# Kernel optimization log

Hardware: AMD Instinct MI355X
Metric: run time of the kernel (lower is better)

## Reference

```python
import jax, jax.numpy as jnp
import numpy as np

L = 2      # decoder layers
B = 4      # batch
T = 1000   # seq_len (mask built for this length)
C = 768    # input_dim / d_model
H = 12     # num_heads
DK = C // H
WIN = 100


def layernorm(x, g, b):
    m = x.mean(-1, keepdims=True)
    v = x.var(-1, keepdims=True)
    return (x - m) / jnp.sqrt(v + 1e-5) * g + b


def pos_encoding(t, c):
    # Transformer-XL / espnet RelPositionalEncoding table: relative positions t-1 .. -(t-1)
    rel = jnp.arange(t - 1, -t, -1, dtype=jnp.float32)          # (2t-1,)
    div = jnp.exp(-jnp.arange(0, c, 2, dtype=jnp.float32) * (np.log(10000.0) / c))
    ang = rel[:, None] * div[None, :]                            # (2t-1, c/2)
    pe = jnp.zeros((2 * t - 1, c), dtype=jnp.float32)
    pe = pe.at[:, 0::2].set(jnp.sin(ang)).at[:, 1::2].set(jnp.cos(ang))
    return pe


def rel_shift(x):
    # x: (B, H, T, 2T-1) -> (B, H, T, T), Transformer-XL relative shift
    b, h, t, p = x.shape
    xp = jnp.pad(x, ((0, 0), (0, 0), (0, 0), (1, 0)))
    xp = xp.reshape(b, h, p + 1, t)[:, :, 1:, :].reshape(b, h, t, p)
    return xp[..., :t]


def setup_inputs() -> dict:
    key = jax.random.key(0)
    ks = jax.random.split(key, 16)
    s = 0.02
    inp = {
        "x": jax.random.normal(ks[0], (B, T, C), dtype=jnp.float32),
        "Wq": jax.random.normal(ks[1], (L, C, C), dtype=jnp.float32) * s,
        "bq": jnp.zeros((L, C), dtype=jnp.float32),
        "Wk": jax.random.normal(ks[2], (L, C, C), dtype=jnp.float32) * s,
        "bk": jnp.zeros((L, C), dtype=jnp.float32),
        "Wv": jax.random.normal(ks[3], (L, C, C), dtype=jnp.float32) * s,
        "bv": jnp.zeros((L, C), dtype=jnp.float32),
        "Wo": jax.random.normal(ks[4], (L, C, C), dtype=jnp.float32) * s,
        "bo": jnp.zeros((L, C), dtype=jnp.float32),
        "Wp": jax.random.normal(ks[5], (L, C, C), dtype=jnp.float32) * s,   # linear_pos, no bias
        "pos_u": jax.random.normal(ks[6], (L, H, DK), dtype=jnp.float32) * s,
        "pos_v": jax.random.normal(ks[7], (L, H, DK), dtype=jnp.float32) * s,
        "ln1_g": jnp.ones((L, C), dtype=jnp.float32),
        "ln1_b": jnp.zeros((L, C), dtype=jnp.float32),
        "ln2_g": jnp.ones((L, C), dtype=jnp.float32),
        "ln2_b": jnp.zeros((L, C), dtype=jnp.float32),
        "W1": jax.random.normal(ks[8], (L, C, C), dtype=jnp.float32) * s,   # mlp_ratio = 1
        "b1": jnp.zeros((L, C), dtype=jnp.float32),
        "W2": jax.random.normal(ks[9], (L, C, C), dtype=jnp.float32) * s,
        "b2": jnp.zeros((L, C), dtype=jnp.float32),
    }
    # diagonal (banded) mask: True = blocked outside the attention window
    i = np.arange(T)
    blocked = np.abs(i[:, None] - i[None, :]) > (WIN // 2)
    inp["att_mask"] = jnp.asarray(blocked)
    return inp


def reference(x, att_mask, Wq, bq, Wk, bk, Wv, bv, Wo, bo, Wp, pos_u, pos_v,
              ln1_g, ln1_b, ln2_g, ln2_b, W1, b1, W2, b2):
    Bb, t, c = x.shape
    pe = pos_encoding(t, c)                       # (2T-1, C)
    h = x * jnp.sqrt(jnp.float32(c))              # xscale in RelPositionalEncoding
    for l in range(L):
        y = layernorm(h, ln1_g[l], ln1_b[l])
        q = (y @ Wq[l] + bq[l]).reshape(Bb, t, H, DK)
        k = (y @ Wk[l] + bk[l]).reshape(Bb, t, H, DK)
        v = (y @ Wv[l] + bv[l]).reshape(Bb, t, H, DK)
        p = (pe @ Wp[l]).reshape(2 * t - 1, H, DK)
        ac = jnp.einsum('bthd,bshd->bhts', q + pos_u[l], k)
        bd = rel_shift(jnp.einsum('bthd,phd->bhtp', q + pos_v[l], p))
        scores = (ac + bd) / jnp.sqrt(jnp.float32(DK))
        scores = jnp.where(att_mask[None, None], jnp.float32(-1e9), scores)
        attn = jax.nn.softmax(scores, axis=-1)
        o = jnp.einsum('bhts,bshd->bthd', attn, v).reshape(Bb, t, c)
        h = h + (o @ Wo[l] + bo[l])
        y2 = layernorm(h, ln2_g[l], ln2_b[l])
        h = h + (jax.nn.gelu(y2 @ W1[l] + b1[l]) @ W2[l] + b2[l])
    return h
```

## Files before the change

kernel.cpp:

```cpp
#include <hip/hip_runtime.h>
#include <math.h>

#define LNUM 2
#define BBATCH 4
#define TSEQ 1000
#define CDIM 768
#define HHEADS 12
#define DKK 64
#define PPOS (2*TSEQ-1)
#define HALFW 50
#define MROWS (BBATCH*TSEQ)
#define MPAD 4096
#define QKVDIM (3*CDIM)
#define NS 176

typedef __attribute__((ext_vector_type(8))) short s16x8;
typedef __attribute__((ext_vector_type(4))) short s16x4;
typedef __attribute__((ext_vector_type(4))) float f32x4;

#define LDSOFF(p) ((unsigned)(uintptr_t)(__attribute__((address_space(3))) const void*)(p))

__device__ __forceinline__ ushort f2bf(float x) {
    unsigned u = __float_as_uint(x);
    unsigned r = u + 0x7FFFu + ((u >> 16) & 1u);
    return (ushort)(r >> 16);
}
__device__ __forceinline__ float bf2f(ushort h) {
    return __uint_as_float(((unsigned)h) << 16);
}
__device__ __forceinline__ float gelu_f(float x) {
    float u = 0.7978845608028654f * (x + 0.044715f * x * x * x);
    return 0.5f * x * (1.f + tanhf(u));
}
__device__ __forceinline__ void gload_lds16(const void* g, void* l) {
    __builtin_amdgcn_global_load_lds(
        (const __attribute__((address_space(1))) void*)g,
        (__attribute__((address_space(3))) void*)l, 16, 0, 0);
}
__device__ __forceinline__ s16x4 tr_read(unsigned addr) {
    s16x4 d;
    asm volatile("ds_read_b64_tr_b16 %0, %1" : "=v"(d) : "v"(addr));
    return d;
}
__device__ __forceinline__ s16x4 tr_read128(unsigned addr) {
    s16x4 d;
    asm volatile("ds_read_b64_tr_b16 %0, %1 offset:128" : "=v"(d) : "v"(addr));
    return d;
}

__global__ __launch_bounds__(256) void transpose_pack(
    const float* __restrict__ Wq, const float* __restrict__ Wk,
    const float* __restrict__ Wv, const float* __restrict__ Wp,
    const float* __restrict__ Wo, const float* __restrict__ W1,
    const float* __restrict__ W2,
    ushort* __restrict__ Wtqkv, ushort* __restrict__ Wtp,
    ushort* __restrict__ Wto, ushort* __restrict__ Wt1, ushort* __restrict__ Wt2) {
    const int l = blockIdx.z / 7, m = blockIdx.z % 7;
    const float* srcs[7] = {Wq, Wk, Wv, Wp, Wo, W1, W2};
    const float* src = srcs[m] + (size_t)l * CDIM * CDIM;
    ushort* dst;
    if (m < 3)       dst = Wtqkv + (size_t)l * QKVDIM * CDIM + (size_t)m * CDIM * CDIM;
    else if (m == 3) dst = Wtp + (size_t)l * CDIM * CDIM;
    else if (m == 4) dst = Wto + (size_t)l * CDIM * CDIM;
    else if (m == 5) dst = Wt1 + (size_t)l * CDIM * CDIM;
    else             dst = Wt2 + (size_t)l * CDIM * CDIM;
    __shared__ float tile[32][33];
    const int tx = threadIdx.x, ty = threadIdx.y;
    const int c0 = blockIdx.x * 32, r0 = blockIdx.y * 32;
#pragma unroll
    for (int i = 0; i < 4; ++i)
        tile[ty + i * 8][tx] = src[(size_t)(r0 + ty + i * 8) * CDIM + c0 + tx];
    __syncthreads();
#pragma unroll
    for (int i = 0; i < 4; ++i)
        dst[(size_t)(c0 + ty + i * 8) * CDIM + r0 + tx] = f2bf(tile[tx][ty + i * 8]);
}

__global__ __launch_bounds__(256) void prep_small(ushort* __restrict__ pe,
                                                  const float* __restrict__ bq,
                                                  const float* __restrict__ bk,
                                                  const float* __restrict__ bv,
                                                  float* __restrict__ bqkv) {
    int idx = blockIdx.x * 256 + threadIdx.x;
    const int npair = 256 * (CDIM / 2);
    if (idx < npair) {
        int jloc = idx / (CDIM / 2);
        int m = idx - jloc * (CDIM / 2);
        int j = 896 + jloc;
        float rel = (float)(TSEQ - 1 - j);
        float div = expf(-(float)(2 * m) * (9.210340371976184f / (float)CDIM));
        float a = rel * div;
        pe[(size_t)j * CDIM + 2 * m]     = f2bf(sinf(a));
        pe[(size_t)j * CDIM + 2 * m + 1] = f2bf(cosf(a));
    }
    if (idx < LNUM * QKVDIM) {
        int l = idx / QKVDIM, c = idx - l * QKVDIM;
        float v;
        if (c < CDIM)            v = bq[l * CDIM + c];
        else if (c < 2 * CDIM)   v = bk[l * CDIM + c - CDIM];
        else                     v = bv[l * CDIM + c - 2 * CDIM];
        bqkv[idx] = v;
    }
}

__global__ __launch_bounds__(192) void ln_kernel(const float* __restrict__ in,
                                                 const float* __restrict__ g,
                                                 const float* __restrict__ bta,
                                                 ushort* __restrict__ y, float xscale) {
    const int row = blockIdx.x, tid = threadIdx.x;
    float4 v = *(const float4*)&in[(size_t)row * CDIM + tid * 4];
    v.x *= xscale; v.y *= xscale; v.z *= xscale; v.w *= xscale;
    float s  = v.x + v.y + v.z + v.w;
    float ss = v.x * v.x + v.y * v.y + v.z * v.z + v.w * v.w;
#pragma unroll
    for (int off = 32; off; off >>= 1) {
        s  += __shfl_xor(s, off);
        ss += __shfl_xor(ss, off);
    }
    __shared__ float sm[3], sq[3];
    const int wid = tid >> 6, lane = tid & 63;
    if (lane == 0) { sm[wid] = s; sq[wid] = ss; }
    __syncthreads();
    const float st  = sm[0] + sm[1] + sm[2];
    const float sst = sq[0] + sq[1] + sq[2];
    const float mean = st * (1.f / CDIM);
    const float var  = sst * (1.f / CDIM) - mean * mean;
    const float rstd = rsqrtf(var + 1e-5f);
    const float4 g4 = *(const float4*)&g[tid * 4];
    const float4 b4 = *(const float4*)&bta[tid * 4];
    ushort o0 = f2bf((v.x - mean) * rstd * g4.x + b4.x);
    ushort o1 = f2bf((v.y - mean) * rstd * g4.y + b4.y);
    ushort o2 = f2bf((v.z - mean) * rstd * g4.z + b4.z);
    ushort o3 = f2bf((v.w - mean) * rstd * g4.w + b4.w);
    uint2 pk; pk.x = (unsigned)o0 | ((unsigned)o1 << 16);
    pk.y = (unsigned)o2 | ((unsigned)o3 << 16);
    *(uint2*)&y[(size_t)row * CDIM + tid * 4] = pk;
}

template <int EPI>
__global__ __launch_bounds__(256, 3) void gemm64(const ushort* __restrict__ A,
                                                 const ushort* __restrict__ Bt,
                                                 const float* __restrict__ bias,
                                                 void* Out, int M, int ldo,
                                                 const float* resid, float rscale,
                                                 size_t zsB, size_t zsO) {
    __shared__ ushort lds[24576];
    const int tid = threadIdx.x;
    const int w = tid >> 6, lane = tid & 63;
    const int row0 = blockIdx.x * 64, col0 = blockIdx.y * 128;
    const size_t zb = blockIdx.z;
    Bt += zb * zsB;
    if (EPI == 2) Out = (void*)((float*)Out + zb * zsO);
    else          Out = (void*)((ushort*)Out + zb * zsO);

    const int srow8  = lane >> 3;
    const int schunk = (lane & 7) ^ srow8;

#define STAGE64(buf, k0)                                                        \
    {                                                                           \
        _Pragma("unroll")                                                       \
        for (int g = 0; g < 6; ++g) {                                           \
            const int grp = w * 6 + g;                                          \
            const int r = grp * 8 + srow8;                                      \
            const ushort* src = (grp < 8)                                       \
                ? A  + (size_t)(row0 + r) * CDIM + (k0) + schunk * 8            \
                : Bt + (size_t)(col0 + (r - 64)) * CDIM + (k0) + schunk * 8;    \
            gload_lds16(src, (char*)lds + (buf) * 24576 + grp * 1024);          \
        }                                                                       \
    }

    const int wm = (w >> 1) * 32, wn = (w & 1) * 64;
    const int lr = lane & 15, q = lane >> 4;
    f32x4 acc[2][4] = {};

    STAGE64(0, 0);
    __syncthreads();
    int cur = 0;
    for (int k0 = 0; k0 < CDIM; k0 += 64) {
        if (k0 + 64 < CDIM) STAGE64(cur ^ 1, k0 + 64);
        const int base = cur * 12288;
#pragma unroll
        for (int kk = 0; kk < 2; ++kk) {
            s16x8 af[2], bfr[4];
#pragma unroll
            for (int i = 0; i < 2; ++i) {
                const int r = wm + i * 16 + lr;
                af[i] = *(const s16x8*)&lds[base + r * 64 + ((((kk << 2) | q) ^ (r & 7)) << 3)];
            }
#pragma unroll
            for (int j = 0; j < 4; ++j) {
                const int r = 64 + wn + j * 16 + lr;
                bfr[j] = *(const s16x8*)&lds[base + r * 64 + ((((kk << 2) | q) ^ (r & 7)) << 3)];
            }
#pragma unroll
            for (int i = 0; i < 2; ++i)
#pragma unroll
                for (int j = 0; j < 4; ++j)
                    acc[i][j] = __builtin_amdgcn_mfma_f32_16x16x32_bf16(af[i], bfr[j], acc[i][j], 0, 0, 0);
        }
        __syncthreads();
        cur ^= 1;
    }
#undef STAGE64

    const int lrr = (lane >> 4) * 4;
    const int lc = lane & 15;
#pragma unroll
    for (int j = 0; j < 4; ++j) {
        const int col = col0 + wn + j * 16 + lc;
        const float bv = bias ? bias[col] : 0.f;
#pragma unroll
        for (int i = 0; i < 2; ++i) {
#pragma unroll
            for (int r = 0; r < 4; ++r) {
                const int row = row0 + wm + i * 16 + lrr + r;
                if (row >= M) continue;
                const float v = acc[i][j][r] + bv;
                if (EPI == 0)
                    ((ushort*)Out)[(size_t)row * ldo + col] = f2bf(v);
                else if (EPI == 1)
                    ((ushort*)Out)[(size_t)row * ldo + col] = f2bf(gelu_f(v));
                else {
                    float* p = (float*)Out + (size_t)row * ldo + col;
                    *p = resid[(size_t)row * ldo + col] * rscale + v;
                }
            }
        }
    }
}

__global__ __launch_bounds__(256, 3) void attn_mfma(
    const ushort* __restrict__ qkv, const ushort* __restrict__ pb,
    const float* __restrict__ pos_u, const float* __restrict__ pos_v,
    ushort* __restrict__ o) {
    __shared__ __align__(16) char smem[51200];
    ushort* Kl   = (ushort*)smem;
    ushort* Pl   = (ushort*)smem;
    ushort* Vsub = (ushort*)(smem + 25600);
    ushort* Bd   = (ushort*)(smem + 37888);

    const int tid = threadIdx.x;
    const int w = tid >> 6, lane = tid & 63;
    const int t0 = blockIdx.x * 64;
    const int h = blockIdx.y, b = blockIdx.z;
    const int m0 = w * 16;
    const int lr = lane & 15, lk = (lane >> 4) * 8, q = lane >> 4;

    auto vsrc = [&](int sp) -> const ushort* {
        const int ob = sp * 1024 + lane * 16;
        const int d0c = ob / 6144;
        const int rem = ob - d0c * 6144;
        const int j = rem >> 5;
        const int halfo = (rem & 31) >> 4;
        int t = t0 - HALFW + j; t = t < 0 ? 0 : (t < TSEQ ? t : TSEQ - 1);
        return qkv + (size_t)(b * TSEQ + t) * QKVDIM + 2 * CDIM + h * DKK
               + (d0c & 1) * 16 + halfo * 8;
    };

    int tq = t0 + m0 + lr; tq = tq < TSEQ ? tq : TSEQ - 1;
    const ushort* qp = qkv + (size_t)(b * TSEQ + tq) * QKVDIM + h * DKK;
    s16x8 qr0 = *(const s16x8*)(qp + lk);
    s16x8 qr1 = *(const s16x8*)(qp + 32 + lk);
    const float* puB = pos_u + h * DKK;
    const float* pvB = pos_v + h * DKK;
    float puA[16], pvA[16];
    *(float4*)&puA[0]  = *(const float4*)(puB + lk);
    *(float4*)&puA[4]  = *(const float4*)(puB + lk + 4);
    *(float4*)&puA[8]  = *(const float4*)(puB + 32 + lk);
    *(float4*)&puA[12] = *(const float4*)(puB + 32 + lk + 4);
    *(float4*)&pvA[0]  = *(const float4*)(pvB + lk);
    *(float4*)&pvA[4]  = *(const float4*)(pvB + lk + 4);
    *(float4*)&pvA[8]  = *(const float4*)(pvB + 32 + lk);
    *(float4*)&pvA[12] = *(const float4*)(pvB + 32 + lk + 4);

    const ushort* pbh = pb + (size_t)949 * CDIM + h * DKK;
    s16x8 pfr[7][2];
#pragma unroll
    for (int uf = 0; uf < 7; ++uf) {
        pfr[uf][0] = *(const s16x8*)&pbh[(size_t)(uf * 16 + lr) * CDIM + lk];
        pfr[uf][1] = *(const s16x8*)&pbh[(size_t)(uf * 16 + lr) * CDIM + 32 + lk];
    }

#pragma unroll
    for (int g = 0; g < 3; ++g) {
        const int sp = w * 3 + g;
        gload_lds16(vsrc(sp), (char*)Vsub + sp * 1024);
    }

    {
        const int srow8 = lane >> 3;
        const int schunk = (lane & 7) ^ srow8;
#pragma unroll
        for (int g = 0; g < 6; ++g) {
            const int sp = w * 6 + g;
            if (sp < 22) {
                const int r = sp * 8 + srow8;
                int kb = t0 - HALFW + r; kb = kb < 0 ? 0 : (kb < TSEQ ? kb : TSEQ - 1);
                const ushort* src = qkv + (size_t)(b * TSEQ + kb) * QKVDIM + CDIM
                                    + h * DKK + schunk * 8;
                gload_lds16(src, (char*)Kl + sp * 1024);
            }
        }
    }

    s16x8 qu0, qu1, qv0, qv1;
#pragma unroll
    for (int e = 0; e < 8; ++e) {
        const float q0 = bf2f((ushort)qr0[e]), q1 = bf2f((ushort)qr1[e]);
        qu0[e] = (short)f2bf(q0 + puA[e]);
        qu1[e] = (short)f2bf(q1 + puA[8 + e]);
        qv0[e] = (short)f2bf(q0 + pvA[e]);
        qv1[e] = (short)f2bf(q1 + pvA[8 + e]);
    }
    __syncthreads();

    const f32x4 zero = {0.f, 0.f, 0.f, 0.f};
    f32x4 acS[11], acB[7];
    __builtin_amdgcn_s_setprio(1);
#pragma unroll
    for (int uf = 0; uf < 7; ++uf) {
        acB[uf] = __builtin_amdgcn_mfma_f32_16x16x32_bf16(qv0, pfr[uf][0], zero, 0, 0, 0);
        acB[uf] = __builtin_amdgcn_mfma_f32_16x16x32_bf16(qv1, pfr[uf][1], acB[uf], 0, 0, 0);
    }
#pragma unroll
    for (int jf = 0; jf < 11; ++jf) {
        const int rr = jf * 16 + lr;
        const int sw = rr & 7;
        s16x8 k0 = *(const s16x8*)&Kl[rr * 64 + (((q)     ^ sw) << 3)];
        s16x8 k1 = *(const s16x8*)&Kl[rr * 64 + (((q | 4) ^ sw) << 3)];
        acS[jf] = __builtin_amdgcn_mfma_f32_16x16x32_bf16(qu0, k0, zero, 0, 0, 0);
        acS[jf] = __builtin_amdgcn_mfma_f32_16x16x32_bf16(qu1, k1, acS[jf], 0, 0, 0);
    }
    __builtin_amdgcn_s_setprio(0);

    ushort* bdw = Bd + w * 16 * 104;
#pragma unroll
    for (int uf = 0; uf < 7; ++uf)
#pragma unroll
        for (int r = 0; r < 4; ++r)
            bdw[((lane >> 4) * 4 + r) * 104 + uf * 16 + lr] = f2bf(acB[uf][r]);
    float mx[4] = {-1e30f, -1e30f, -1e30f, -1e30f};
#pragma unroll
    for (int jf = 0; jf < 11; ++jf)
#pragma unroll
        for (int r = 0; r < 4; ++r) {
            const int tl = (lane >> 4) * 4 + r;
            const int tloc = m0 + tl;
            const int j = jf * 16 + lr;
            const int u = j - tloc;
            const int s = t0 - HALFW + j;
            const bool valid = (u >= 0) & (u <= 2 * HALFW) & (s >= 0) & (s < TSEQ)
                               & (t0 + tloc < TSEQ);
            float sc = -1e30f;
            if (valid) sc = (acS[jf][r] + bf2f(bdw[tl * 104 + u])) * 0.125f;
            acS[jf][r] = sc;
            mx[r] = fmaxf(mx[r], sc);
        }
#pragma unroll
    for (int r = 0; r < 4; ++r)
#pragma unroll
        for (int off = 8; off; off >>= 1)
            mx[r] = fmaxf(mx[r], __shfl_xor(mx[r], off));
    float sm[4] = {0.f, 0.f, 0.f, 0.f};
#pragma unroll
    for (int jf = 0; jf < 11; ++jf)
#pragma unroll
        for (int r = 0; r < 4; ++r) {
            float e = __expf(acS[jf][r] - mx[r]);
            acS[jf][r] = e;
            sm[r] += e;
        }
#pragma unroll
    for (int r = 0; r < 4; ++r) {
#pragma unroll
        for (int off = 8; off; off >>= 1) sm[r] += __shfl_xor(sm[r], off);
        sm[r] = 1.f / sm[r];
    }
    __syncthreads();

    s16x8 vr0 = *vsrc(12 + w * 3 + 0);
    s16x8 vr1 = *vsrc(12 + w * 3 + 1);
    s16x8 vr2 = *vsrc(12 + w * 3 + 2);

#pragma unroll
    for (int jf = 0; jf < 11; ++jf)
#pragma unroll
        for (int r = 0; r < 4; ++r)
            Pl[(m0 + (lane >> 4) * 4 + r) * 200 + jf * 16 + lr] = f2bf(acS[jf][r]);
#pragma unroll
    for (int r = 0; r < 4; ++r)
        Pl[(m0 + (lane >> 4) * 4 + r) * 200 + 176 + lr] = 0;

    s16x8 pa[6];
#pragma unroll
    for (int ks = 0; ks < 6; ++ks)
        pa[ks] = *(const s16x8*)&Pl[(m0 + lr) * 200 + ks * 32 + lk];

    const unsigned vbase = LDSOFF(Vsub);
#pragma unroll
    for (int nf = 0; nf < 2; ++nf) {
        const unsigned abase = vbase + (nf & 1) * 6144 + ((lane >> 4) << 8) + ((lane & 15) << 1);
        s16x4 lo[6], hi[6];
#pragma unroll
        for (int ks = 0; ks < 6; ++ks) {
            lo[ks] = tr_read(abase + ks * 1024);
            hi[ks] = tr_read128(abase + ks * 1024);
        }
        asm volatile("s_waitcnt lgkmcnt(0)" ::: "memory");
        __builtin_amdgcn_sched_barrier(0);
        f32x4 acO = {};
        __builtin_amdgcn_s_setprio(1);
#pragma unroll
        for (int ks = 0; ks < 6; ++ks) {
            s16x8 vb = __builtin_shufflevector(lo[ks], hi[ks], 0, 1, 2, 3, 4, 5, 6, 7);
            acO = __builtin_amdgcn_mfma_f32_16x16x32_bf16(pa[ks], vb, acO, 0, 0, 0);
        }
        __builtin_amdgcn_s_setprio(0);
#pragma unroll
        for (int r = 0; r < 4; ++r) {
            const int t = t0 + m0 + (lane >> 4) * 4 + r;
            if (t < TSEQ)
                o[(size_t)(b * TSEQ + t) * CDIM + h * DKK + nf * 16 + lr] =
                    f2bf(acO[r] * sm[r]);
        }
    }
    __syncthreads();

    *(s16x8*)((char*)Vsub + (w * 3 + 0) * 1024 + lane * 16) = vr0;
    *(s16x8*)((char*)Vsub + (w * 3 + 1) * 1024 + lane * 16) = vr1;
    *(s16x8*)((char*)Vsub + (w * 3 + 2) * 1024 + lane * 16) = vr2;
    __syncthreads();

#pragma unroll
    for (int nf = 2; nf < 4; ++nf) {
        const unsigned abase = vbase + (nf & 1) * 6144 + ((lane >> 4) << 8) + ((lane & 15) << 1);
        s16x4 lo[6], hi[6];
#pragma unroll
        for (int ks = 0; ks < 6; ++ks) {
            lo[ks] = tr_read(abase + ks * 1024);
            hi[ks] = tr_read128(abase + ks * 1024);
        }
        asm volatile("s_waitcnt lgkmcnt(0)" ::: "memory");
        __builtin_amdgcn_sched_barrier(0);
        f32x4 acO = {};
        __builtin_amdgcn_s_setprio(1);
#pragma unroll
        for (int ks = 0; ks < 6; ++ks) {
            s16x8 vb = __builtin_shufflevector(lo[ks], hi[ks], 0, 1, 2, 3, 4, 5, 6, 7);
            acO = __builtin_amdgcn_mfma_f32_16x16x32_bf16(pa[ks], vb, acO, 0, 0, 0);
        }
        __builtin_amdgcn_s_setprio(0);
#pragma unroll
        for (int r = 0; r < 4; ++r) {
            const int t = t0 + m0 + (lane >> 4) * 4 + r;
            if (t < TSEQ)
                o[(size_t)(b * TSEQ + t) * CDIM + h * DKK + nf * 16 + lr] =
                    f2bf(acO[r] * sm[r]);
        }
    }
}

extern "C" void kernel_launch(void* const* d_in, const int* in_sizes, int n_in,
                              void* d_out, int out_size, void* d_ws, size_t ws_size,
                              hipStream_t stream) {
    const float* x     = (const float*)d_in[0];
    const float* Wq    = (const float*)d_in[1];
    const float* bq    = (const float*)d_in[2];
    const float* Wk    = (const float*)d_in[3];
    const float* bk    = (const float*)d_in[4];
    const float* Wv    = (const float*)d_in[5];
    const float* bv    = (const float*)d_in[6];
    const float* Wo    = (const float*)d_in[7];
    const float* bo    = (const float*)d_in[8];
    const float* Wp    = (const float*)d_in[9];
    const float* pos_u = (const float*)d_in[10];
    const float* pos_v = (const float*)d_in[11];
    const float* ln1g  = (const float*)d_in[12];
    const float* ln1b  = (const float*)d_in[13];
    const float* ln2g  = (const float*)d_in[14];
    const float* ln2b  = (const float*)d_in[15];
    const float* W1    = (const float*)d_in[16];
    const float* b1    = (const float*)d_in[17];
    const float* W2    = (const float*)d_in[18];
    const float* b2    = (const float*)d_in[19];

    float* h = (float*)d_out;
    const float XS = 27.712812921102035f;

    char* p = (char*)d_ws;
    ushort* Wtqkv = (ushort*)p;               p += (size_t)LNUM * QKVDIM * CDIM * 2;
    ushort* Wtp   = (ushort*)p;               p += (size_t)LNUM * CDIM * CDIM * 2;
    ushort* Wto   = (ushort*)p;               p += (size_t)LNUM * CDIM * CDIM * 2;
    ushort* Wt1   = (ushort*)p;               p += (size_t)LNUM * CDIM * CDIM * 2;
    ushort* Wt2   = (ushort*)p;               p += (size_t)LNUM * CDIM * CDIM * 2;
    float*  bqkv  = (float*)p;                p += (size_t)LNUM * QKVDIM * 4;
    ushort* pe    = (ushort*)p;               p += (size_t)2048 * CDIM * 2;
    ushort* pb    = (ushort*)p;               p += (size_t)LNUM * 2048 * CDIM * 2;
    ushort* y     = (ushort*)p;               p += (size_t)MPAD * CDIM * 2;
    ushort* qkv   = (ushort*)p;               p += (size_t)MPAD * QKVDIM * 2;
    ushort* o     = (ushort*)p;               p += (size_t)MPAD * CDIM * 2;
    ushort* hid   = (ushort*)p;               p += (size_t)MPAD * CDIM * 2;

    transpose_pack<<<dim3(24, 24, LNUM * 7), dim3(32, 8), 0, stream>>>(
        Wq, Wk, Wv, Wp, Wo, W1, W2, Wtqkv, Wtp, Wto, Wt1, Wt2);
    prep_small<<<384, 256, 0, stream>>>(pe, bq, bk, bv, bqkv);

    const int MB = (MROWS + 63) / 64;
    const dim3 gQKV(MB, QKVDIM / 128);
    const dim3 gC(MB, CDIM / 128);
    const dim3 gP(4, CDIM / 128, LNUM);
    const dim3 gA(16, HHEADS, BBATCH);

    gemm64<0><<<gP, 256, 0, stream>>>(pe + (size_t)896 * CDIM, Wtp, nullptr,
                                      pb + (size_t)896 * CDIM, 256, CDIM,
                                      nullptr, 0.f,
                                      (size_t)CDIM * CDIM, (size_t)2048 * CDIM);

    for (int l = 0; l < LNUM; ++l) {
        const size_t wo = (size_t)l * CDIM * CDIM;
        const float* res1 = (l == 0) ? x : h;
        const float rs1   = (l == 0) ? XS : 1.f;
        ln_kernel<<<MROWS, 192, 0, stream>>>(res1, ln1g + l * CDIM, ln1b + l * CDIM, y, rs1);
        gemm64<0><<<gQKV, 256, 0, stream>>>(y, Wtqkv + (size_t)l * QKVDIM * CDIM,
                                            bqkv + l * QKVDIM, qkv, MROWS, QKVDIM,
                                            nullptr, 0.f, 0, 0);
        attn_mfma<<<gA, 256, 0, stream>>>(
            qkv, pb + (size_t)l * 2048 * CDIM,
            pos_u + l * HHEADS * DKK, pos_v + l * HHEADS * DKK, o);
        gemm64<2><<<gC, 256, 0, stream>>>(o, Wto + wo, bo + l * CDIM, h, MROWS, CDIM,
                                          res1, rs1, 0, 0);
        ln_kernel<<<MROWS, 192, 0, stream>>>(h, ln2g + l * CDIM, ln2b + l * CDIM, y, 1.f);
        gemm64<1><<<gC, 256, 0, stream>>>(y, Wt1 + wo, b1 + l * CDIM, hid, MROWS, CDIM,
                                          nullptr, 0.f, 0, 0);
        gemm64<2><<<gC, 256, 0, stream>>>(hid, Wt2 + wo, b2 + l * CDIM, h, MROWS, CDIM,
                                          h, 1.f, 0, 0);
    }
}
```

Baseline: 261.5 us.

## Replace GEMM with 128x128 tile, 5-stage pipeline, XCD swizzle; fuse prep kernels

The 64x128 double-buffered GEMM is replaced by a 128x128 tile with BK=32 and a 5-slot LDS ring, keeping four stages in flight through manual vmcnt waits and raw barriers. Block indices are remapped so neighbouring tiles land on the same XCD, which should improve L2 reuse. The prep_small kernel is folded into transpose_pack as an extra z-slice, and the transpose now uses float4 loads and packed stores. In attention, the positional-fragment global loads are moved after the Q preparation. The larger tile roughly halves the grid (e.g. 32x6 blocks for the C-wide GEMMs), so occupancy and wave balance across CUs may suffer.

```diff
diff --git a/kernel.cpp b/kernel.cpp
--- a/kernel.cpp
+++ b/kernel.cpp
@@ -13,6 +13,7 @@
 #define MPAD 4096
 #define QKVDIM (3*CDIM)
 #define NS 176
+#define NSTEP (CDIM/32)
 
 typedef __attribute__((ext_vector_type(8))) short s16x8;
 typedef __attribute__((ext_vector_type(4))) short s16x4;
@@ -46,6 +47,11 @@
     s16x4 d;
     asm volatile("ds_read_b64_tr_b16 %0, %1 offset:128" : "=v"(d) : "v"(addr));
     return d;
+}
+__device__ __forceinline__ int xcd_swz(int orig, int nwg) {
+    const int xcd = orig & 7, ixc = orig >> 3;
+    const int qq = nwg >> 3, rr = nwg & 7;
+    return (xcd < rr ? xcd * (qq + 1) : rr * (qq + 1) + (xcd - rr) * qq) + ixc;
 }
 
 __global__ __launch_bounds__(256) void transpose_pack(
@@ -54,7 +60,35 @@
     const float* __restrict__ Wo, const float* __restrict__ W1,
     const float* __restrict__ W2,
     ushort* __restrict__ Wtqkv, ushort* __restrict__ Wtp,
-    ushort* __restrict__ Wto, ushort* __restrict__ Wt1, ushort* __restrict__ Wt2) {
+    ushort* __restrict__ Wto, ushort* __restrict__ Wt1, ushort* __restrict__ Wt2,
+    ushort* __restrict__ pe,
+    const float* __restrict__ bq, const float* __restrict__ bk,
+    const float* __restrict__ bv, float* __restrict__ bqkv) {
+    const int tx = threadIdx.x, ty = threadIdx.y;
+    if (blockIdx.z == 14) {
+        const int linear = blockIdx.y * 24 + blockIdx.x;
+        const int idx = linear * 256 + ty * 8 + tx;
+        const int npair = 256 * (CDIM / 2);
+        if (idx < npair) {
+            int jloc = idx / (CDIM / 2);
+            int m = idx - jloc * (CDIM / 2);
+            int j = 896 + jloc;
+            float rel = (float)(TSEQ - 1 - j);
+            float div = expf(-(float)(2 * m) * (9.210340371976184f / (float)CDIM));
+            float a = rel * div;
+            pe[(size_t)j * CDIM + 2 * m]     = f2bf(sinf(a));
+            pe[(size_t)j * CDIM + 2 * m + 1] = f2bf(cosf(a));
+        }
+        if (idx < LNUM * QKVDIM) {
+            int l = idx / QKVDIM, c = idx - l * QKVDIM;
+            float v;
+            if (c < CDIM)            v = bq[l * CDIM + c];
+            else if (c < 2 * CDIM)   v = bk[l * CDIM + c - CDIM];
+            else                     v = bv[l * CDIM + c - 2 * CDIM];
+            bqkv[idx] = v;
+        }
+        return;
+    }
     const int l = blockIdx.z / 7, m = blockIdx.z % 7;
     const float* srcs[7] = {Wq, Wk, Wv, Wp, Wo, W1, W2};
     const float* src = srcs[m] + (size_t)l * CDIM * CDIM;
@@ -65,42 +99,19 @@
     else if (m == 5) dst = Wt1 + (size_t)l * CDIM * CDIM;
     else             dst = Wt2 + (size_t)l * CDIM * CDIM;
     __shared__ float tile[32][33];
-    const int tx = threadIdx.x, ty = threadIdx.y;
     const int c0 = blockIdx.x * 32, r0 = blockIdx.y * 32;
-#pragma unroll
-    for (int i = 0; i < 4; ++i)
-        tile[ty + i * 8][tx] = src[(size_t)(r0 + ty + i * 8) * CDIM + c0 + tx];
+    const float4 v = *(const float4*)&src[(size_t)(r0 + ty) * CDIM + c0 + tx * 4];
+    tile[tx * 4 + 0][ty] = v.x;
+    tile[tx * 4 + 1][ty] = v.y;
+    tile[tx * 4 + 2][ty] = v.z;
+    tile[tx * 4 + 3][ty] = v.w;
     __syncthreads();
-#pragma unroll
-    for (int i = 0; i < 4; ++i)
-        dst[(size_t)(c0 + ty + i * 8) * CDIM + r0 + tx] = f2bf(tile[tx][ty + i * 8]);
-}
-
-__global__ __launch_bounds__(256) void prep_small(ushort* __restrict__ pe,
-                                                  const float* __restrict__ bq,
-                                                  const float* __restrict__ bk,
-                                                  const float* __restrict__ bv,
-                                                  float* __restrict__ bqkv) {
-    int idx = blockIdx.x * 256 + threadIdx.x;
-    const int npair = 256 * (CDIM / 2);
-    if (idx < npair) {
-        int jloc = idx / (CDIM / 2);
-        int m = idx - jloc * (CDIM / 2);
-        int j = 896 + jloc;
-        float rel = (float)(TSEQ - 1 - j);
-        float div = expf(-(float)(2 * m) * (9.210340371976184f / (float)CDIM));
-        float a = rel * div;
-        pe[(size_t)j * CDIM + 2 * m]     = f2bf(sinf(a));
-        pe[(size_t)j * CDIM + 2 * m + 1] = f2bf(cosf(a));
-    }
-    if (idx < LNUM * QKVDIM) {
-        int l = idx / QKVDIM, c = idx - l * QKVDIM;
-        float v;
-        if (c < CDIM)            v = bq[l * CDIM + c];
-        else if (c < 2 * CDIM)   v = bk[l * CDIM + c - CDIM];
-        else                     v = bv[l * CDIM + c - 2 * CDIM];
-        bqkv[idx] = v;
-    }
+    const float a0 = tile[ty][tx * 4 + 0], a1 = tile[ty][tx * 4 + 1];
+    const float a2 = tile[ty][tx * 4 + 2], a3 = tile[ty][tx * 4 + 3];
+    uint2 pk;
+    pk.x = (unsigned)f2bf(a0) | ((unsigned)f2bf(a1) << 16);
+    pk.y = (unsigned)f2bf(a2) | ((unsigned)f2bf(a3) << 16);
+    *(uint2*)&dst[(size_t)(c0 + ty) * CDIM + r0 + tx * 4] = pk;
 }
 
 __global__ __launch_bounds__(192) void ln_kernel(const float* __restrict__ in,
@@ -138,82 +149,84 @@
 }
 
 template <int EPI>
-__global__ __launch_bounds__(256, 3) void gemm64(const ushort* __restrict__ A,
-                                                 const ushort* __restrict__ Bt,
-                                                 const float* __restrict__ bias,
-                                                 void* Out, int M, int ldo,
-                                                 const float* resid, float rscale,
-                                                 size_t zsB, size_t zsO) {
-    __shared__ ushort lds[24576];
+__global__ __launch_bounds__(256, 2) void gemm128d(const ushort* __restrict__ A,
+                                                   const ushort* __restrict__ Bt,
+                                                   const float* __restrict__ bias,
+                                                   void* Out, int M, int ldo,
+                                                   const float* resid, float rscale,
+                                                   size_t zsB, size_t zsO) {
+    __shared__ ushort lds[5 * 8192];
     const int tid = threadIdx.x;
     const int w = tid >> 6, lane = tid & 63;
-    const int row0 = blockIdx.x * 64, col0 = blockIdx.y * 128;
-    const size_t zb = blockIdx.z;
-    Bt += zb * zsB;
-    if (EPI == 2) Out = (void*)((float*)Out + zb * zsO);
-    else          Out = (void*)((ushort*)Out + zb * zsO);
-
-    const int srow8  = lane >> 3;
-    const int schunk = (lane & 7) ^ srow8;
-
-#define STAGE64(buf, k0)                                                        \
-    {                                                                           \
-        _Pragma("unroll")                                                       \
-        for (int g = 0; g < 6; ++g) {                                           \
-            const int grp = w * 6 + g;                                          \
-            const int r = grp * 8 + srow8;                                      \
-            const ushort* src = (grp < 8)                                       \
-                ? A  + (size_t)(row0 + r) * CDIM + (k0) + schunk * 8            \
-                : Bt + (size_t)(col0 + (r - 64)) * CDIM + (k0) + schunk * 8;    \
-            gload_lds16(src, (char*)lds + (buf) * 24576 + grp * 1024);          \
-        }                                                                       \
-    }
-
-    const int wm = (w >> 1) * 32, wn = (w & 1) * 64;
+    const int nwg = gridDim.x * gridDim.y;
+    const int newid = xcd_swz(blockIdx.y * gridDim.x + blockIdx.x, nwg);
+    const int col0 = (newid % gridDim.y) * 128;
+    const int row0 = (newid / gridDim.y) * 128;
+    Bt += blockIdx.z * zsB;
+    if (EPI == 2) Out = (void*)((float*)Out + blockIdx.z * zsO);
+    else          Out = (void*)((ushort*)Out + blockIdx.z * zsO);
+    const int srow   = lane >> 2;
+    const int schunk = (lane & 3) ^ ((lane >> 3) & 3);
+    const int wm = (w >> 1) * 64, wn = (w & 1) * 64;
     const int lr = lane & 15, q = lane >> 4;
-    f32x4 acc[2][4] = {};
-
-    STAGE64(0, 0);
-    __syncthreads();
-    int cur = 0;
-    for (int k0 = 0; k0 < CDIM; k0 += 64) {
-        if (k0 + 64 < CDIM) STAGE64(cur ^ 1, k0 + 64);
-        const int base = cur * 12288;
-#pragma unroll
-        for (int kk = 0; kk < 2; ++kk) {
-            s16x8 af[2], bfr[4];
-#pragma unroll
-            for (int i = 0; i < 2; ++i) {
-                const int r = wm + i * 16 + lr;
-                af[i] = *(const s16x8*)&lds[base + r * 64 + ((((kk << 2) | q) ^ (r & 7)) << 3)];
-            }
-#pragma unroll
-            for (int j = 0; j < 4; ++j) {
-                const int r = 64 + wn + j * 16 + lr;
-                bfr[j] = *(const s16x8*)&lds[base + r * 64 + ((((kk << 2) | q) ^ (r & 7)) << 3)];
-            }
-#pragma unroll
-            for (int i = 0; i < 2; ++i)
-#pragma unroll
-                for (int j = 0; j < 4; ++j)
-                    acc[i][j] = __builtin_amdgcn_mfma_f32_16x16x32_bf16(af[i], bfr[j], acc[i][j], 0, 0, 0);
-        }
-        __syncthreads();
-        cur ^= 1;
-    }
-#undef STAGE64
-
+
+#define STG(s)                                                                   \
+    {                                                                            \
+        _Pragma("unroll")                                                        \
+        for (int g = 0; g < 4; ++g) {                                            \
+            const int sp = w * 4 + g;                                            \
+            const int r = sp * 16 + srow;                                        \
+            const ushort* src = (r < 128)                                        \
+                ? A  + (size_t)(row0 + r) * CDIM + (s) * 32 + schunk * 8         \
+                : Bt + (size_t)(col0 + (r - 128)) * CDIM + (s) * 32 + schunk * 8;\
+            gload_lds16(src, (char*)lds + ((s) % 5) * 16384 + sp * 1024);        \
+        }                                                                        \
+    }
+
+    f32x4 acc[4][4] = {};
+    STG(0); STG(1); STG(2); STG(3);
+    for (int t = 0; t < NSTEP; ++t) {
+        if (t < NSTEP - 3)       asm volatile("s_waitcnt vmcnt(12)" ::: "memory");
+        else if (t == NSTEP - 3) asm volatile("s_waitcnt vmcnt(8)" ::: "memory");
+        else if (t == NSTEP - 2) asm volatile("s_waitcnt vmcnt(4)" ::: "memory");
+        else                     asm volatile("s_waitcnt vmcnt(0)" ::: "memory");
+        __builtin_amdgcn_sched_barrier(0);
+        __builtin_amdgcn_s_barrier();
+        __builtin_amdgcn_sched_barrier(0);
+        if (t + 4 < NSTEP) STG(t + 4);
+        const int base = (t % 5) * 8192;
+        s16x8 af[4], bfr[4];
+#pragma unroll
+        for (int i = 0; i < 4; ++i) {
+            const int r = wm + i * 16 + lr;
+            af[i] = *(const s16x8*)&lds[base + r * 32 + ((q ^ ((r >> 1) & 3)) << 3)];
+        }
+#pragma unroll
+        for (int j = 0; j < 4; ++j) {
+            const int r = 128 + wn + j * 16 + lr;
+            bfr[j] = *(const s16x8*)&lds[base + r * 32 + ((q ^ ((r >> 1) & 3)) << 3)];
+        }
+#pragma unroll
+        for (int i = 0; i < 4; ++i)
+#pragma unroll
+            for (int j = 0; j < 4; ++j)
+                acc[i][j] = __builtin_amdgcn_mfma_f32_16x16x32_bf16(af[i], bfr[j], acc[i][j], 0, 0, 0);
+    }
+#undef STG
+
+    const int crow0 = row0 + (w >> 1) * 64;
+    const int ccol0 = col0 + (w & 1) * 64;
     const int lrr = (lane >> 4) * 4;
     const int lc = lane & 15;
 #pragma unroll
     for (int j = 0; j < 4; ++j) {
-        const int col = col0 + wn + j * 16 + lc;
+        const int col = ccol0 + j * 16 + lc;
         const float bv = bias ? bias[col] : 0.f;
 #pragma unroll
-        for (int i = 0; i < 2; ++i) {
+        for (int i = 0; i < 4; ++i) {
 #pragma unroll
             for (int r = 0; r < 4; ++r) {
-                const int row = row0 + wm + i * 16 + lrr + r;
+                const int row = crow0 + i * 16 + lrr + r;
                 if (row >= M) continue;
                 const float v = acc[i][j][r] + bv;
                 if (EPI == 0)
@@ -273,20 +286,11 @@
     *(float4*)&pvA[8]  = *(const float4*)(pvB + 32 + lk);
     *(float4*)&pvA[12] = *(const float4*)(pvB + 32 + lk + 4);
 
-    const ushort* pbh = pb + (size_t)949 * CDIM + h * DKK;
-    s16x8 pfr[7][2];
-#pragma unroll
-    for (int uf = 0; uf < 7; ++uf) {
-        pfr[uf][0] = *(const s16x8*)&pbh[(size_t)(uf * 16 + lr) * CDIM + lk];
-        pfr[uf][1] = *(const s16x8*)&pbh[(size_t)(uf * 16 + lr) * CDIM + 32 + lk];
-    }
-
 #pragma unroll
     for (int g = 0; g < 3; ++g) {
         const int sp = w * 3 + g;
         gload_lds16(vsrc(sp), (char*)Vsub + sp * 1024);
     }
-
     {
         const int srow8 = lane >> 3;
         const int schunk = (lane & 7) ^ srow8;
@@ -311,6 +315,14 @@
         qu1[e] = (short)f2bf(q1 + puA[8 + e]);
         qv0[e] = (short)f2bf(q0 + pvA[e]);
         qv1[e] = (short)f2bf(q1 + pvA[8 + e]);
+    }
+
+    const ushort* pbh = pb + (size_t)949 * CDIM + h * DKK;
+    s16x8 pfr[7][2];
+#pragma unroll
+    for (int uf = 0; uf < 7; ++uf) {
+        pfr[uf][0] = *(const s16x8*)&pbh[(size_t)(uf * 16 + lr) * CDIM + lk];
+        pfr[uf][1] = *(const s16x8*)&pbh[(size_t)(uf * 16 + lr) * CDIM + 32 + lk];
     }
     __syncthreads();
 
@@ -501,38 +513,37 @@
     ushort* o     = (ushort*)p;               p += (size_t)MPAD * CDIM * 2;
     ushort* hid   = (ushort*)p;               p += (size_t)MPAD * CDIM * 2;
 
-    transpose_pack<<<dim3(24, 24, LNUM * 7), dim3(32, 8), 0, stream>>>(
-        Wq, Wk, Wv, Wp, Wo, W1, W2, Wtqkv, Wtp, Wto, Wt1, Wt2);
-    prep_small<<<384, 256, 0, stream>>>(pe, bq, bk, bv, bqkv);
-
-    const int MB = (MROWS + 63) / 64;
-    const dim3 gQKV(MB, QKVDIM / 128);
-    const dim3 gC(MB, CDIM / 128);
-    const dim3 gP(4, CDIM / 128, LNUM);
+    transpose_pack<<<dim3(24, 24, 15), dim3(8, 32), 0, stream>>>(
+        Wq, Wk, Wv, Wp, Wo, W1, W2, Wtqkv, Wtp, Wto, Wt1, Wt2,
+        pe, bq, bk, bv, bqkv);
+
+    const dim3 gQKV(32, QKVDIM / 128);
+    const dim3 gC(32, CDIM / 128);
+    const dim3 gP(2, CDIM / 128, LNUM);
     const dim3 gA(16, HHEADS, BBATCH);
 
-    gemm64<0><<<gP, 256, 0, stream>>>(pe + (size_t)896 * CDIM, Wtp, nullptr,
-                                      pb + (size_t)896 * CDIM, 256, CDIM,
-                                      nullptr, 0.f,
-                                      (size_t)CDIM * CDIM, (size_t)2048 * CDIM);
+    gemm128d<0><<<gP, 256, 0, stream>>>(pe + (size_t)896 * CDIM, Wtp, nullptr,
+                                        pb + (size_t)896 * CDIM, 256, CDIM,
+                                        nullptr, 0.f,
+                                        (size_t)CDIM * CDIM, (size_t)2048 * CDIM);
 
     for (int l = 0; l < LNUM; ++l) {
         const size_t wo = (size_t)l * CDIM * CDIM;
         const float* res1 = (l == 0) ? x : h;
         const float rs1   = (l == 0) ? XS : 1.f;
         ln_kernel<<<MROWS, 192, 0, stream>>>(res1, ln1g + l * CDIM, ln1b + l * CDIM, y, rs1);
-        gemm64<0><<<gQKV, 256, 0, stream>>>(y, Wtqkv + (size_t)l * QKVDIM * CDIM,
-                                            bqkv + l * QKVDIM, qkv, MROWS, QKVDIM,
-                                            nullptr, 0.f, 0, 0);
+        gemm128d<0><<<gQKV, 256, 0, stream>>>(y, Wtqkv + (size_t)l * QKVDIM * CDIM,
+                                              bqkv + l * QKVDIM, qkv, MROWS, QKVDIM,
+                                              nullptr, 0.f, 0, 0);
         attn_mfma<<<gA, 256, 0, stream>>>(
             qkv, pb + (size_t)l * 2048 * CDIM,
             pos_u + l * HHEADS * DKK, pos_v + l * HHEADS * DKK, o);
-        gemm64<2><<<gC, 256, 0, stream>>>(o, Wto + wo, bo + l * CDIM, h, MROWS, CDIM,
-                                          res1, rs1, 0, 0);
+        gemm128d<2><<<gC, 256, 0, stream>>>(o, Wto + wo, bo + l * CDIM, h, MROWS, CDIM,
+                                            res1, rs1, 0, 0);
         ln_kernel<<<MROWS, 192, 0, stream>>>(h, ln2g + l * CDIM, ln2b + l * CDIM, y, 1.f);
-        gemm64<1><<<gC, 256, 0, stream>>>(y, Wt1 + wo, b1 + l * CDIM, hid, MROWS, CDIM,
-                                          nullptr, 0.f, 0, 0);
-        gemm64<2><<<gC, 256, 0, stream>>>(hid, Wt2 + wo, b2 + l * CDIM, h, MROWS, CDIM,
-                                          h, 1.f, 0, 0);
-    }
-}
+        gemm128d<1><<<gC, 256, 0, stream>>>(y, Wt1 + wo, b1 + l * CDIM, hid, MROWS, CDIM,
+                                            nullptr, 0.f, 0, 0);
+        gemm128d<2><<<gC, 256, 0, stream>>>(hid, Wt2 + wo, b2 + l * CDIM, h, MROWS, CDIM,
+                                            h, 1.f, 0, 0);
+    }
+}
```

After: 347.3 us. +32.8%, slower.
